# Optimization experiments

Measured on AMD Instinct MI355X. Metric: run time of the kernel, lower is better.

Reference implementation:

```python
import jax, jax.numpy as jnp
import numpy as np

NUM_HEADS = 8
BN_EPS = 1e-5


def _conv3x3(x, w, B, N, s):
    # x: (B, N, 3*s*s). Torch loops conv2d per batch element; equivalent to one
    # conv over the flattened (B*N, 3, s, s) batch.
    xi = x.reshape(B * N, 3, s, s)
    y = jax.lax.conv_general_dilated(
        xi, w, window_strides=(1, 1), padding='SAME',
        dimension_numbers=('NCHW', 'OIHW', 'NCHW'))
    return y.reshape(B, N, 3 * s * s)


def setup_inputs() -> dict:
    key = jax.random.key(0)
    ks = jax.random.split(key, 8)
    B, N, C, s = 4, 1024, 768, 16
    H = NUM_HEADS
    q = jax.random.normal(ks[0], (B, N, C), jnp.float32)
    k = jax.random.normal(ks[1], (B, N, C), jnp.float32)
    v = jax.random.normal(ks[2], (B, N, C), jnp.float32)
    qw = jax.random.normal(ks[3], (3, 3, 3, 3), jnp.float32) * 0.1
    kw = jax.random.normal(ks[4], (3, 3, 3, 3), jnp.float32) * 0.1
    vw = jax.random.normal(ks[5], (3, 3, 3, 3), jnp.float32) * 0.1
    rw = jax.random.normal(ks[6], (H, H), jnp.float32) * 0.3  # Conv2d(H,H,1,1) weight
    rb = jnp.zeros((H,), jnp.float32)
    bn_gamma = jnp.ones((H,), jnp.float32)
    bn_beta = jnp.zeros((H,), jnp.float32)
    pw = jax.random.normal(ks[7], (C, C), jnp.float32) * 0.02
    pb = jnp.zeros((C,), jnp.float32)
    return dict(q=q, k=k, v=v, qw=qw, kw=kw, vw=vw, rw=rw, rb=rb,
                bn_gamma=bn_gamma, bn_beta=bn_beta, pw=pw, pb=pb)


def reference(q, k, v, qw, kw, vw, rw, rb, bn_gamma, bn_beta, pw, pb):
    B, N, C = q.shape
    H = NUM_HEADS
    d = C // H
    s = int(np.sqrt(C // 3))
    scale = d ** -0.5
    # conv-projected q/k/v, back to (B, N, C)
    qc = _conv3x3(q, qw, B, N, s)
    kc = _conv3x3(k, kw, B, N, s)
    vc = _conv3x3(v, vw, B, N, s)
    # split heads: (B, H, N, d)
    qh = qc.reshape(B, N, H, d).transpose(0, 2, 1, 3)
    kh = kc.reshape(B, N, H, d).transpose(0, 2, 1, 3)
    vh = vc.reshape(B, N, H, d).transpose(0, 2, 1, 3)
    attn = jax.nn.softmax(jnp.einsum('bhnd,bhmd->bhnm', qh, kh) * scale, axis=-1)
    # re-attention: 1x1 cross-head conv + BatchNorm2d(H) in eval mode
    # (running_mean=0, running_var=1); reatten_scale = 1.0
    attn = jnp.einsum('bhnm,gh->bgnm', attn, rw) + rb[None, :, None, None]
    attn = attn * (bn_gamma / jnp.sqrt(1.0 + BN_EPS))[None, :, None, None] \
           + bn_beta[None, :, None, None]
    x = jnp.einsum('bhnm,bhmd->bhnd', attn, vh)
    x = x.transpose(0, 2, 1, 3).reshape(B, N, C)
    return x @ pw.T + pb
```

## Files before the change

kernel.cpp:

```cpp
#include <hip/hip_runtime.h>
#include <hip/hip_bf16.h>
#include <math.h>

#define B 4
#define N 1024
#define C 768
#define H 8
#define D 96

typedef _Float16 half8 __attribute__((ext_vector_type(8)));
typedef _Float16 half4 __attribute__((ext_vector_type(4)));
typedef float f32x4 __attribute__((ext_vector_type(4)));

#define BN_RSQ 0.9999950000374997f
#define QK_SCALE 0.10206207261596577f

__global__ __launch_bounds__(256) void conv_tok(const float* __restrict__ x,
                                                const float* __restrict__ w,
                                                _Float16* __restrict__ out) {
    __shared__ float sx[768];
    __shared__ float sw[81];
    int t = blockIdx.x;
    const float* xt = x + (size_t)t * 768;
    int tid = threadIdx.x;
    sx[tid]       = xt[tid];
    sx[tid + 256] = xt[tid + 256];
    sx[tid + 512] = xt[tid + 512];
    if (tid < 81) sw[tid] = w[tid];
    __syncthreads();
    int i = tid >> 4, j = tid & 15;
    float acc0 = 0.f, acc1 = 0.f, acc2 = 0.f;
    #pragma unroll
    for (int c = 0; c < 3; ++c) {
        #pragma unroll
        for (int di = 0; di < 3; ++di) {
            int ii = i + di - 1;
            if (ii < 0 || ii > 15) continue;
            #pragma unroll
            for (int dj = 0; dj < 3; ++dj) {
                int jj = j + dj - 1;
                if (jj < 0 || jj > 15) continue;
                float xv = sx[c * 256 + ii * 16 + jj];
                acc0 += xv * sw[(0 * 3 + c) * 9 + di * 3 + dj];
                acc1 += xv * sw[(1 * 3 + c) * 9 + di * 3 + dj];
                acc2 += xv * sw[(2 * 3 + c) * 9 + di * 3 + dj];
            }
        }
    }
    _Float16* ot = out + (size_t)t * 768;
    ot[0 * 256 + tid] = (_Float16)acc0;
    ot[1 * 256 + tid] = (_Float16)acc1;
    ot[2 * 256 + tid] = (_Float16)acc2;
}

__global__ __launch_bounds__(256) void transpose_v(const _Float16* __restrict__ vcH,
                                                   _Float16* __restrict__ vcT) {
    __shared__ _Float16 tile[64][66];
    int n0 = blockIdx.x * 64, c0 = blockIdx.y * 64, b = blockIdx.z;
    int tid = threadIdx.x;
    for (int i = tid; i < 4096; i += 256) {
        int r = i >> 6, c = i & 63;
        tile[r][c] = vcH[((size_t)(b * N + n0 + r)) * C + c0 + c];
    }
    __syncthreads();
    for (int i = tid; i < 4096; i += 256) {
        int cr = i >> 6, nc = i & 63;
        vcT[((size_t)(b * 768 + c0 + cr)) * N + n0 + nc] = tile[nc][cr];
    }
}

__global__ __launch_bounds__(256) void vsum_row(const _Float16* __restrict__ vcT,
                                                float* __restrict__ vsum) {
    int row = blockIdx.x * 4 + (threadIdx.x >> 6);
    int lane = threadIdx.x & 63;
    const _Float16* p = vcT + (size_t)row * N;
    float s = 0.f;
    #pragma unroll
    for (int it = 0; it < 2; ++it) {
        half8 v = *(const half8*)(p + (it * 64 + lane) * 8);
        #pragma unroll
        for (int i = 0; i < 8; ++i) s += (float)v[i];
    }
    #pragma unroll
    for (int off = 1; off < 64; off <<= 1) s += __shfl_xor(s, off);
    if (lane == 0) vsum[row] = s;
}

__global__ __launch_bounds__(256) void lrow_mfma(const _Float16* __restrict__ qcH,
                                                 const _Float16* __restrict__ kcH,
                                                 float* __restrict__ Lrow) {
    __shared__ __align__(16) char smem[49152];
    char* Qb = smem;
    char* Kb = smem + 24576;
    const int n0 = blockIdx.x * 128, z = blockIdx.y;
    const int b = z >> 3, h = z & 7;
    const int tid = threadIdx.x;
    const _Float16* qg = qcH + ((size_t)(b * N + n0)) * C + h * D;
    const _Float16* kgb = kcH + ((size_t)(b * N)) * C + h * D;
    #pragma unroll
    for (int it = 0; it < 6; ++it) {
        int chunk = it * 256 + tid;
        int r = chunk / 12, cc = (chunk - r * 12) * 8;
        half8 qv = *(const half8*)(qg + (size_t)r * C + cc);
        *(half8*)(Qb + (((r * 96 + cc) * 2) ^ ((r & 7) << 4))) = qv;
    }
    const int wid = tid >> 6, lane = tid & 63;
    const int wr = wid >> 1, wc = wid & 1;
    const int l15 = lane & 15, l4 = lane >> 4;
    float rs[4][4] = {};
    for (int m0 = 0; m0 < 1024; m0 += 128) {
        __syncthreads();
        #pragma unroll
        for (int it = 0; it < 6; ++it) {
            int chunk = it * 256 + tid;
            int r = chunk / 12, cc = (chunk - r * 12) * 8;
            half8 kv = *(const half8*)(kgb + (size_t)(m0 + r) * C + cc);
            *(half8*)(Kb + (((r * 96 + cc) * 2) ^ ((r & 7) << 4))) = kv;
        }
        __syncthreads();
        f32x4 acc[4][4] = {};
        #pragma unroll
        for (int ks = 0; ks < 3; ++ks) {
            int k0 = ks * 32 + l4 * 8;
            half8 a[4], bf[4];
            #pragma unroll
            for (int fm = 0; fm < 4; ++fm) {
                int row = wr * 64 + fm * 16 + l15;
                a[fm] = *(half8*)(Qb + (((row * 96 + k0) * 2) ^ ((row & 7) << 4)));
            }
            #pragma unroll
            for (int fn = 0; fn < 4; ++fn) {
                int row = wc * 64 + fn * 16 + l15;
                bf[fn] = *(half8*)(Kb + (((row * 96 + k0) * 2) ^ ((row & 7) << 4)));
            }
            #pragma unroll
            for (int fm = 0; fm < 4; ++fm)
                #pragma unroll
                for (int fn = 0; fn < 4; ++fn)
                    acc[fm][fn] = __builtin_amdgcn_mfma_f32_16x16x32_f16(a[fm], bf[fn], acc[fm][fn], 0, 0, 0);
        }
        #pragma unroll
        for (int fm = 0; fm < 4; ++fm)
            #pragma unroll
            for (int j = 0; j < 4; ++j) {
                float s = 0.f;
                #pragma unroll
                for (int fn = 0; fn < 4; ++fn)
                    s += __expf(acc[fm][fn][j] * QK_SCALE);
                rs[fm][j] += s;
            }
    }
    #pragma unroll
    for (int fm = 0; fm < 4; ++fm)
        #pragma unroll
        for (int j = 0; j < 4; ++j) {
            float s = rs[fm][j];
            s += __shfl_xor(s, 1);
            s += __shfl_xor(s, 2);
            s += __shfl_xor(s, 4);
            s += __shfl_xor(s, 8);
            if (l15 == 0)
                atomicAdd(&Lrow[z * N + n0 + wr * 64 + fm * 16 + l4 * 4 + j], s);
        }
}

__global__ __launch_bounds__(512) void mixpv(const _Float16* __restrict__ qcH,
                                             const _Float16* __restrict__ kcH,
                                             const _Float16* __restrict__ vcT,
                                             const float* __restrict__ Lrow,
                                             const float* __restrict__ rw,
                                             const float* __restrict__ gamma,
                                             float* __restrict__ x) {
    __shared__ __align__(16) _Float16 P[8 * 32 * 64];
    __shared__ float w2s[64];
    const int n0 = blockIdx.x * 32;
    const int msbase = blockIdx.y * 512;
    const int b = blockIdx.z;
    const int tid = threadIdx.x;
    if (tid < 64) {
        int g = tid >> 3, hh = tid & 7;
        w2s[tid] = gamma[g] * BN_RSQ * rw[g * 8 + hh];
    }
    const int n_t = tid >> 4;
    const int mq4 = (tid & 15) * 4;
    float IL[8];
    #pragma unroll
    for (int h = 0; h < 8; ++h)
        IL[h] = 1.0f / Lrow[(size_t)(b * 8 + h) * N + n0 + n_t];
    const int wid = tid >> 6, lane = tid & 63;
    const int l15 = lane & 15, l4 = lane >> 4;
    char* Pb = (char*)P;
    half8 q8[2][3];
    #pragma unroll
    for (int fm = 0; fm < 2; ++fm)
        #pragma unroll
        for (int ks = 0; ks < 3; ++ks)
            q8[fm][ks] = *(const half8*)(qcH + (size_t)(b * N + n0 + fm * 16 + l15) * C
                                         + wid * 96 + ks * 32 + l4 * 8);
    __syncthreads();
    f32x4 acc_u[2][6] = {};
    for (int mt = 0; mt < 8; ++mt) {
        const int m0 = msbase + mt * 64;
        #pragma unroll
        for (int fn = 0; fn < 4; ++fn) {
            half8 kf[3];
            #pragma unroll
            for (int ks = 0; ks < 3; ++ks)
                kf[ks] = *(const half8*)(kcH + (size_t)(b * N + m0 + fn * 16 + l15) * C
                                         + wid * 96 + ks * 32 + l4 * 8);
            f32x4 a4[2] = {};
            #pragma unroll
            for (int ks = 0; ks < 3; ++ks)
                #pragma unroll
                for (int fm = 0; fm < 2; ++fm)
                    a4[fm] = __builtin_amdgcn_mfma_f32_16x16x32_f16(q8[fm][ks], kf[ks], a4[fm], 0, 0, 0);
            #pragma unroll
            for (int fm = 0; fm < 2; ++fm)
                #pragma unroll
                for (int j = 0; j < 4; ++j) {
                    float p = __expf(a4[fm][j] * QK_SCALE);
                    int n = fm * 16 + l4 * 4 + j;
                    int m = fn * 16 + l15;
                    *(_Float16*)(Pb + wid * 4096 + ((n * 128 + m * 2) ^ ((n & 7) << 4))) = (_Float16)p;
                }
        }
        __syncthreads();
        {
            f32x4 vmix[8] = {};
            #pragma unroll
            for (int h = 0; h < 8; ++h) {
                half4 p4 = *(half4*)(Pb + h * 4096 + ((n_t * 128 + mq4 * 2) ^ ((n_t & 7) << 4)));
                f32x4 pq;
                #pragma unroll
                for (int i = 0; i < 4; ++i) pq[i] = (float)p4[i] * IL[h];
                #pragma unroll
                for (int g = 0; g < 8; ++g) {
                    float wv = w2s[g * 8 + h];
                    #pragma unroll
                    for (int i = 0; i < 4; ++i) vmix[g][i] += wv * pq[i];
                }
            }
            #pragma unroll
            for (int g = 0; g < 8; ++g) {
                half4 hv;
                #pragma unroll
                for (int i = 0; i < 4; ++i) hv[i] = (_Float16)vmix[g][i];
                *(half4*)(Pb + g * 4096 + ((n_t * 128 + mq4 * 2) ^ ((n_t & 7) << 4))) = hv;
            }
        }
        __syncthreads();
        #pragma unroll
        for (int ks2 = 0; ks2 < 2; ++ks2) {
            half8 af[2];
            #pragma unroll
            for (int fm = 0; fm < 2; ++fm) {
                int n = fm * 16 + l15;
                af[fm] = *(half8*)(Pb + wid * 4096 + ((n * 128 + (ks2 * 32 + l4 * 8) * 2) ^ ((n & 7) << 4)));
            }
            #pragma unroll
            for (int fn2 = 0; fn2 < 6; ++fn2) {
                half8 vf = *(const half8*)(vcT + (size_t)(b * 768 + wid * 96 + fn2 * 16 + l15) * N
                                           + m0 + ks2 * 32 + l4 * 8);
                #pragma unroll
                for (int fm = 0; fm < 2; ++fm)
                    acc_u[fm][fn2] = __builtin_amdgcn_mfma_f32_16x16x32_f16(af[fm], vf, acc_u[fm][fn2], 0, 0, 0);
            }
        }
        __syncthreads();
    }
    #pragma unroll
    for (int fm = 0; fm < 2; ++fm)
        #pragma unroll
        for (int fn2 = 0; fn2 < 6; ++fn2)
            #pragma unroll
            for (int j = 0; j < 4; ++j) {
                int n = n0 + fm * 16 + l4 * 4 + j;
                int c = wid * 96 + fn2 * 16 + l15;
                atomicAdd(&x[((size_t)(b * N + n)) * C + c], acc_u[fm][fn2][j]);
            }
}

__global__ __launch_bounds__(256) void proj_mfma(const float* __restrict__ x,
                                                 const float* __restrict__ vsum,
                                                 const float* __restrict__ pw,
                                                 const float* __restrict__ pb,
                                                 const float* __restrict__ rb,
                                                 const float* __restrict__ gamma,
                                                 const float* __restrict__ beta,
                                                 float* __restrict__ out) {
    __shared__ _Float16 sX[128 * 32];
    __shared__ _Float16 sW[96 * 32];
    const int t0 = blockIdx.x * 128, c0 = blockIdx.y * 96;
    const int b = t0 >> 10;
    const int tid = threadIdx.x;
    const int wid = tid >> 6, lane = tid & 63;
    const int wr = wid >> 1, wc = wid & 1;
    const int l15 = lane & 15, l4 = lane >> 4;
    char* Xb = (char*)sX;
    char* Wb = (char*)sW;
    f32x4 acc[4][3] = {};
    for (int k0 = 0; k0 < 768; k0 += 32) {
        __syncthreads();
        #pragma unroll
        for (int it = 0; it < 4; ++it) {
            int q = it * 256 + tid;
            int r = q >> 3, c4 = (q & 7) * 4;
            f32x4 xv = *(const f32x4*)(x + (size_t)(t0 + r) * C + k0 + c4);
            int g = (k0 + c4) / 96;
            float cg = gamma[g] * BN_RSQ * rb[g] + beta[g];
            const f32x4 vs = *(const f32x4*)(vsum + b * 768 + k0 + c4);
            half4 hv;
            #pragma unroll
            for (int i = 0; i < 4; ++i) hv[i] = (_Float16)(xv[i] + cg * vs[i]);
            *(half4*)(Xb + (((r * 32 + c4) * 2) ^ ((r & 7) << 4))) = hv;
        }
        #pragma unroll
        for (int it = 0; it < 3; ++it) {
            int q = it * 256 + tid;
            int r = q >> 3, c4 = (q & 7) * 4;
            f32x4 wv = *(const f32x4*)(pw + (size_t)(c0 + r) * C + k0 + c4);
            half4 hv;
            #pragma unroll
            for (int i = 0; i < 4; ++i) hv[i] = (_Float16)wv[i];
            *(half4*)(Wb + (((r * 32 + c4) * 2) ^ ((r & 7) << 4))) = hv;
        }
        __syncthreads();
        half8 af[4];
        #pragma unroll
        for (int fm = 0; fm < 4; ++fm) {
            int r = wr * 64 + fm * 16 + l15;
            af[fm] = *(half8*)(Xb + (((r * 32 + l4 * 8) * 2) ^ ((r & 7) << 4)));
        }
        #pragma unroll
        for (int fn = 0; fn < 3; ++fn) {
            int r = wc * 48 + fn * 16 + l15;
            half8 bf = *(half8*)(Wb + (((r * 32 + l4 * 8) * 2) ^ ((r & 7) << 4)));
            #pragma unroll
            for (int fm = 0; fm < 4; ++fm)
                acc[fm][fn] = __builtin_amdgcn_mfma_f32_16x16x32_f16(af[fm], bf, acc[fm][fn], 0, 0, 0);
        }
    }
    #pragma unroll
    for (int fm = 0; fm < 4; ++fm)
        #pragma unroll
        for (int fn = 0; fn < 3; ++fn) {
            int cc = c0 + wc * 48 + fn * 16 + l15;
            float bias = pb[cc];
            #pragma unroll
            for (int j = 0; j < 4; ++j) {
                int t = t0 + wr * 64 + fm * 16 + l4 * 4 + j;
                out[(size_t)t * C + cc] = acc[fm][fn][j] + bias;
            }
        }
}

extern "C" void kernel_launch(void* const* d_in, const int* in_sizes, int n_in,
                              void* d_out, int out_size, void* d_ws, size_t ws_size,
                              hipStream_t stream) {
    const float* q     = (const float*)d_in[0];
    const float* k     = (const float*)d_in[1];
    const float* v     = (const float*)d_in[2];
    const float* qw    = (const float*)d_in[3];
    const float* kw    = (const float*)d_in[4];
    const float* vw    = (const float*)d_in[5];
    const float* rw    = (const float*)d_in[6];
    const float* rb    = (const float*)d_in[7];
    const float* gamma = (const float*)d_in[8];
    const float* beta  = (const float*)d_in[9];
    const float* pw    = (const float*)d_in[10];
    const float* pb    = (const float*)d_in[11];
    float* out = (float*)d_out;

    char* ws = (char*)d_ws;
    float*    xacc = (float*)ws;
    _Float16* qcH  = (_Float16*)(ws + 12582912);
    _Float16* kcH  = (_Float16*)(ws + 18874368);
    _Float16* vcH  = (_Float16*)(ws + 25165824);
    _Float16* vcT  = (_Float16*)(ws + 31457280);
    float*    Lrow = (float*)(ws + 37748736);
    float*    vsum = (float*)(ws + 37879808);

    hipMemsetAsync(Lrow, 0, 131072, stream);
    hipMemsetAsync(xacc, 0, 12582912, stream);

    conv_tok<<<dim3(B * N), dim3(256), 0, stream>>>(q, qw, qcH);
    conv_tok<<<dim3(B * N), dim3(256), 0, stream>>>(k, kw, kcH);
    conv_tok<<<dim3(B * N), dim3(256), 0, stream>>>(v, vw, vcH);

    transpose_v<<<dim3(16, 12, B), dim3(256), 0, stream>>>(vcH, vcT);
    vsum_row<<<dim3(768), dim3(256), 0, stream>>>(vcT, vsum);

    lrow_mfma<<<dim3(8, 32), dim3(256), 0, stream>>>(qcH, kcH, Lrow);

    mixpv<<<dim3(32, 2, B), dim3(512), 0, stream>>>(qcH, kcH, vcT, Lrow, rw, gamma, xacc);

    proj_mfma<<<dim3(32, 8), dim3(256), 0, stream>>>(xacc, vsum, pw, pb, rb, gamma, beta, out);
}
```

Measured before the change: 273.7 us.

## Fuse conv launches, split key range for more blocks, packed fp16 head mixing

Merges the three per-tensor conv launches into one grid. lrow_mfma and mixpv each split the key dimension further (to 512 and 256 keys per block), doubling their block counts, with a block-id remap so neighbouring blocks share a batch/head. The cross-head mixing in mixpv now runs in packed half2 arithmetic with weights precomputed once by a small kernel. This targets launch overhead, low occupancy on many CUs and the scalar fp32 mixing loop, at the cost of fp16 accumulation precision and more atomic adds into the shared accumulators.

```diff
diff --git a/kernel.cpp b/kernel.cpp
--- a/kernel.cpp
+++ b/kernel.cpp
@@ -10,14 +10,39 @@
 
 typedef _Float16 half8 __attribute__((ext_vector_type(8)));
 typedef _Float16 half4 __attribute__((ext_vector_type(4)));
+typedef _Float16 h2 __attribute__((ext_vector_type(2)));
 typedef float f32x4 __attribute__((ext_vector_type(4)));
 
 #define BN_RSQ 0.9999950000374997f
 #define QK_SCALE 0.10206207261596577f
 
-__global__ __launch_bounds__(256) void conv_tok(const float* __restrict__ x,
-                                                const float* __restrict__ w,
-                                                _Float16* __restrict__ out) {
+static __device__ __forceinline__ h2 u32_to_h2(unsigned int u) {
+    union { unsigned int u; h2 h; } c; c.u = u; return c.h;
+}
+
+__global__ __launch_bounds__(64) void w2prep(const float* __restrict__ rw,
+                                             const float* __restrict__ gamma,
+                                             unsigned int* __restrict__ w2pk) {
+    int t = threadIdx.x;
+    int g = t >> 3, h = t & 7;
+    float w = gamma[g] * BN_RSQ * rw[g * 8 + h];
+    union { _Float16 f; unsigned short s; } c; c.f = (_Float16)w;
+    w2pk[t] = (unsigned int)c.s | ((unsigned int)c.s << 16);
+}
+
+__global__ __launch_bounds__(256) void conv_all(const float* __restrict__ q,
+                                                const float* __restrict__ k,
+                                                const float* __restrict__ v,
+                                                const float* __restrict__ qw,
+                                                const float* __restrict__ kw,
+                                                const float* __restrict__ vw,
+                                                _Float16* __restrict__ qo,
+                                                _Float16* __restrict__ ko,
+                                                _Float16* __restrict__ vo) {
+    const int sel = blockIdx.y;
+    const float* x = sel == 0 ? q : sel == 1 ? k : v;
+    const float* w = sel == 0 ? qw : sel == 1 ? kw : vw;
+    _Float16* out = sel == 0 ? qo : sel == 1 ? ko : vo;
     __shared__ float sx[768];
     __shared__ float sw[81];
     int t = blockIdx.x;
@@ -92,7 +117,11 @@
     __shared__ __align__(16) char smem[49152];
     char* Qb = smem;
     char* Kb = smem + 24576;
-    const int n0 = blockIdx.x * 128, z = blockIdx.y;
+    const int id = blockIdx.x;
+    const int z = (id & 7) | (((id >> 3) & 3) << 3);
+    const int r4 = id >> 5;
+    const int n0 = (r4 & 7) * 128;
+    const int mh = r4 >> 3;
     const int b = z >> 3, h = z & 7;
     const int tid = threadIdx.x;
     const _Float16* qg = qcH + ((size_t)(b * N + n0)) * C + h * D;
@@ -108,7 +137,7 @@
     const int wr = wid >> 1, wc = wid & 1;
     const int l15 = lane & 15, l4 = lane >> 4;
     float rs[4][4] = {};
-    for (int m0 = 0; m0 < 1024; m0 += 128) {
+    for (int m0 = mh * 512; m0 < mh * 512 + 512; m0 += 128) {
         __syncthreads();
         #pragma unroll
         for (int it = 0; it < 6; ++it) {
@@ -168,25 +197,25 @@
                                              const _Float16* __restrict__ kcH,
                                              const _Float16* __restrict__ vcT,
                                              const float* __restrict__ Lrow,
-                                             const float* __restrict__ rw,
-                                             const float* __restrict__ gamma,
+                                             const unsigned int* __restrict__ w2pk,
                                              float* __restrict__ x) {
     __shared__ __align__(16) _Float16 P[8 * 32 * 64];
-    __shared__ float w2s[64];
-    const int n0 = blockIdx.x * 32;
-    const int msbase = blockIdx.y * 512;
-    const int b = blockIdx.z;
+    const int gid = blockIdx.x;
+    const int grp = gid & 15;
+    const int b = grp >> 2, qtr = grp & 3;
+    const int n0 = (gid >> 4) * 32;
+    const int msbase = qtr * 256;
     const int tid = threadIdx.x;
-    if (tid < 64) {
-        int g = tid >> 3, hh = tid & 7;
-        w2s[tid] = gamma[g] * BN_RSQ * rw[g * 8 + hh];
-    }
     const int n_t = tid >> 4;
     const int mq4 = (tid & 15) * 4;
-    float IL[8];
-    #pragma unroll
-    for (int h = 0; h < 8; ++h)
-        IL[h] = 1.0f / Lrow[(size_t)(b * 8 + h) * N + n0 + n_t];
+    h2 IL2[8];
+    #pragma unroll
+    for (int h = 0; h < 8; ++h) {
+        float il = 1.0f / Lrow[(size_t)(b * 8 + h) * N + n0 + n_t];
+        _Float16 i16 = (_Float16)il;
+        h2 t; t[0] = i16; t[1] = i16;
+        IL2[h] = t;
+    }
     const int wid = tid >> 6, lane = tid & 63;
     const int l15 = lane & 15, l4 = lane >> 4;
     char* Pb = (char*)P;
@@ -197,9 +226,8 @@
         for (int ks = 0; ks < 3; ++ks)
             q8[fm][ks] = *(const half8*)(qcH + (size_t)(b * N + n0 + fm * 16 + l15) * C
                                          + wid * 96 + ks * 32 + l4 * 8);
-    __syncthreads();
     f32x4 acc_u[2][6] = {};
-    for (int mt = 0; mt < 8; ++mt) {
+    for (int mt = 0; mt < 4; ++mt) {
         const int m0 = msbase + mt * 64;
         #pragma unroll
         for (int fn = 0; fn < 4; ++fn) {
@@ -226,26 +254,27 @@
         }
         __syncthreads();
         {
-            f32x4 vmix[8] = {};
+            h2 pn0[8], pn1[8];
             #pragma unroll
             for (int h = 0; h < 8; ++h) {
                 half4 p4 = *(half4*)(Pb + h * 4096 + ((n_t * 128 + mq4 * 2) ^ ((n_t & 7) << 4)));
-                f32x4 pq;
-                #pragma unroll
-                for (int i = 0; i < 4; ++i) pq[i] = (float)p4[i] * IL[h];
-                #pragma unroll
-                for (int g = 0; g < 8; ++g) {
-                    float wv = w2s[g * 8 + h];
-                    #pragma unroll
-                    for (int i = 0; i < 4; ++i) vmix[g][i] += wv * pq[i];
+                h2 lo; lo[0] = p4[0]; lo[1] = p4[1];
+                h2 hi; hi[0] = p4[2]; hi[1] = p4[3];
+                pn0[h] = lo * IL2[h];
+                pn1[h] = hi * IL2[h];
+            }
+            #pragma unroll
+            for (int g = 0; g < 8; ++g) {
+                h2 a0 = {(_Float16)0.f, (_Float16)0.f};
+                h2 a1 = a0;
+                #pragma unroll
+                for (int h = 0; h < 8; ++h) {
+                    h2 w = u32_to_h2(w2pk[g * 8 + h]);
+                    a0 = w * pn0[h] + a0;
+                    a1 = w * pn1[h] + a1;
                 }
-            }
-            #pragma unroll
-            for (int g = 0; g < 8; ++g) {
-                half4 hv;
-                #pragma unroll
-                for (int i = 0; i < 4; ++i) hv[i] = (_Float16)vmix[g][i];
-                *(half4*)(Pb + g * 4096 + ((n_t * 128 + mq4 * 2) ^ ((n_t & 7) << 4))) = hv;
+                half4 o; o[0] = a0[0]; o[1] = a0[1]; o[2] = a1[0]; o[3] = a1[1];
+                *(half4*)(Pb + g * 4096 + ((n_t * 128 + mq4 * 2) ^ ((n_t & 7) << 4))) = o;
             }
         }
         __syncthreads();
@@ -379,20 +408,21 @@
     _Float16* vcT  = (_Float16*)(ws + 31457280);
     float*    Lrow = (float*)(ws + 37748736);
     float*    vsum = (float*)(ws + 37879808);
+    unsigned int* w2pk = (unsigned int*)(ws + 37892096);
 
     hipMemsetAsync(Lrow, 0, 131072, stream);
     hipMemsetAsync(xacc, 0, 12582912, stream);
 
-    conv_tok<<<dim3(B * N), dim3(256), 0, stream>>>(q, qw, qcH);
-    conv_tok<<<dim3(B * N), dim3(256), 0, stream>>>(k, kw, kcH);
-    conv_tok<<<dim3(B * N), dim3(256), 0, stream>>>(v, vw, vcH);
+    w2prep<<<dim3(1), dim3(64), 0, stream>>>(rw, gamma, w2pk);
+
+    conv_all<<<dim3(B * N, 3), dim3(256), 0, stream>>>(q, k, v, qw, kw, vw, qcH, kcH, vcH);
 
     transpose_v<<<dim3(16, 12, B), dim3(256), 0, stream>>>(vcH, vcT);
     vsum_row<<<dim3(768), dim3(256), 0, stream>>>(vcT, vsum);
 
-    lrow_mfma<<<dim3(8, 32), dim3(256), 0, stream>>>(qcH, kcH, Lrow);
-
-    mixpv<<<dim3(32, 2, B), dim3(512), 0, stream>>>(qcH, kcH, vcT, Lrow, rw, gamma, xacc);
+    lrow_mfma<<<dim3(512), dim3(256), 0, stream>>>(qcH, kcH, Lrow);
+
+    mixpv<<<dim3(512), dim3(512), 0, stream>>>(qcH, kcH, vcT, Lrow, w2pk, xacc);
 
     proj_mfma<<<dim3(32, 8), dim3(256), 0, stream>>>(xacc, vsum, pw, pb, rb, gamma, beta, out);
 }
```

Result: no change. 273.1 us (-0.2%).
